# Kernel tuning notes

Measured on AMD Instinct MI355X. Metric: run time of the kernel, lower is better.

The kernel has to match this reference:

```python
import jax, jax.numpy as jnp
import numpy as np

B, C, H, W = 512, 1, 280, 280
K, S, F = 28, 28, 10           # kernel, stride, nfilters
HS, WS = 10, 10                # output spatial spans (280/28)
SPAN = HS * WS                 # 100 patch locations
OUT = 10                       # out_channels
DEC_IN = HS * WS * F           # 1000


def setup_inputs() -> dict:
    key = jax.random.key(0)
    k1, k2, k3, k4, k5 = jax.random.split(key, 5)
    x = jax.random.normal(k1, (B, C, H, W), dtype=jnp.float32)
    # locally-connected weights: one kernel per (filter, spatial location), torch layout [F*SPAN, C, K, K]
    conv_w = jax.random.normal(k2, (F * SPAN, C, K, K), dtype=jnp.float32) * 0.02
    conv_b = jax.random.normal(k3, (F * SPAN, C), dtype=jnp.float32) * 0.02
    dec_w = jax.random.normal(k4, (OUT, DEC_IN), dtype=jnp.float32) * 0.02
    dec_b = jax.random.normal(k5, (OUT,), dtype=jnp.float32) * 0.02
    return {"x": x, "conv_w": conv_w, "conv_b": conv_b, "dec_w": dec_w, "dec_b": dec_b}


def reference(x, conv_w, conv_b, dec_w, dec_b):
    # Extract non-overlapping KxK patches (stride == kernel_size, padding == 0):
    # [B,C,H,W] -> [B,C,HS,K,WS,K] -> [B,HS,WS,C,K,K] -> [B,SPAN,C,K,K]
    # matches torch unfold(2).unfold(3) ordering (height span outer, width span inner).
    patches = x.reshape(B, C, HS, K, WS, K).transpose(0, 2, 4, 1, 3, 5)
    patches = patches.reshape(B, SPAN, C, K, K)
    # weight index in torch is f*SPAN + s (x is tiled SPAN-fastest by repeat)
    w = conv_w.reshape(F, SPAN, C, K, K)
    # per-location elementwise mul + reduce over (kh, kw) == batched tiny contraction
    out = jnp.einsum('bscij,fscij->bfsc', patches, w)  # [B,F,SPAN,C]
    out = out + conv_b.reshape(F, SPAN, C)
    out = out.reshape(B, F, HS, WS)  # valid since C == 1 (as in torch view)
    out = jax.nn.relu(out).reshape(B, DEC_IN)
    return out @ dec_w.T + dec_b
```

## Files before the change

kernel.cpp:

```cpp
#include <hip/hip_runtime.h>
#include <hip/hip_bf16.h>

#define HW      280
#define IMG     78400
#define KK      28
#define F_N     10
#define SPAN    100
#define OUT_N   10
#define P_PLANE 512000

typedef short s16x8 __attribute__((ext_vector_type(8)));
typedef float f32x4 __attribute__((ext_vector_type(4)));

__global__ __launch_bounds__(256) void wprep(const float* __restrict__ cw,
                                             unsigned* __restrict__ wbuf) {
  const int idx = blockIdx.x * 256 + (int)threadIdx.x;
  const int k2  = idx & 15;
  const int f   = (idx >> 4) & 15;
  const int rs  = idx >> 8;
  const int r   = rs % 28;
  const int s   = rs / 28;
  unsigned out = 0;
  if (f < F_N) {
    const int k0 = k2 * 2, k1 = k0 + 1;
    const float v0 = (k0 < KK) ? cw[(size_t)(f * SPAN + s) * (KK * KK) + r * KK + k0] : 0.f;
    const float v1 = (k1 < KK) ? cw[(size_t)(f * SPAN + s) * (KK * KK) + r * KK + k1] : 0.f;
    __hip_bfloat162 h2 = __float22bfloat162_rn(make_float2(v0, v1));
    out = *reinterpret_cast<unsigned*>(&h2);
  }
  wbuf[idx] = out;
}

__global__ __launch_bounds__(256, 4) void lcn_conv(
    const float* __restrict__ x, const unsigned short* __restrict__ wbuf,
    float* __restrict__ P) {
  const int bid  = blockIdx.x;
  const int xcd  = bid & 7;
  const int grp  = bid >> 3;
  const int hsrq = xcd + 8 * (grp % 5);
  const int bg   = grp / 5;
  const int hs   = hsrq >> 2;
  const int rq   = hsrq & 3;

  const int tid  = (int)threadIdx.x;
  const int lane = tid & 63;
  const int wid  = tid >> 6;
  const int l15  = lane & 15;
  const int kg   = lane >> 4;

  __shared__ short xl[2][16 * 320];

  for (int i = tid; i < 2 * 160; i += 256) {
    const int buf = i / 160, j = i - buf * 160;
    const int b = j / 10, ws = j - b * 10;
    const int sidx = (b * 320 + ws * 32 + 28) ^ ((b & 7) << 3);
    *reinterpret_cast<short4*>(&xl[buf][sidx]) = make_short4(0, 0, 0, 0);
  }

  const int nun = (wid < 2) ? 3 : 2;
  const int wsl[3] = {wid, wid + 4, wid + 8};

  f32x4 acc[3];
#pragma unroll
  for (int u = 0; u < 3; ++u) acc[u] = (f32x4){0.f, 0.f, 0.f, 0.f};

  const int row0 = hs * KK + rq * 7;
  const float* xbase = x + (size_t)bg * 16 * IMG + (size_t)row0 * HW;

  float4 stg[5];
  auto issue = [&](int r) {
#pragma unroll
    for (int j = 0; j < 5; ++j) {
      const int i = tid + 256 * j;
      if (i < 1120) {
        const int b = i / 70, q = i - b * 70;
        stg[j] = *reinterpret_cast<const float4*>(
            xbase + (size_t)b * IMG + (size_t)r * HW + q * 4);
      }
    }
  };
  auto commit = [&](int buf) {
#pragma unroll
    for (int j = 0; j < 5; ++j) {
      const int i = tid + 256 * j;
      if (i < 1120) {
        const int b = i / 70, q = i - b * 70;
        const int ws = q / 7, c4 = q - ws * 7;
        __hip_bfloat162 h0 = __float22bfloat162_rn(make_float2(stg[j].x, stg[j].y));
        __hip_bfloat162 h1 = __float22bfloat162_rn(make_float2(stg[j].z, stg[j].w));
        const int sidx = (b * 320 + ws * 32 + c4 * 4) ^ ((b & 7) << 3);
        uint2 pk;
        pk.x = *reinterpret_cast<unsigned*>(&h0);
        pk.y = *reinterpret_cast<unsigned*>(&h1);
        *reinterpret_cast<uint2*>(&xl[buf][sidx]) = pk;
      }
    }
  };

  issue(0);
  commit(0);
  __syncthreads();

  for (int r = 0; r < 7; ++r) {
    const int buf = r & 1;
    if (r < 6) issue(r + 1);
    const int rr = rq * 7 + r;
#pragma unroll
    for (int u = 0; u < 3; ++u) {
      if (u < nun) {
        const int ws = wsl[u];
        const int s  = hs * 10 + ws;
        const s16x8 bfr = *reinterpret_cast<const s16x8*>(
            wbuf + (size_t)(s * 28 + rr) * 512 + l15 * 32 + kg * 8);
        const int sidx = (l15 * 320 + ws * 32 + kg * 8) ^ ((l15 & 7) << 3);
        const s16x8 afr = *reinterpret_cast<const s16x8*>(&xl[buf][sidx]);
        acc[u] = __builtin_amdgcn_mfma_f32_16x16x32_bf16(afr, bfr, acc[u], 0, 0, 0);
      }
    }
    if (r < 6) commit(buf ^ 1);
    __syncthreads();
  }

  if (l15 < F_N) {
#pragma unroll
    for (int u = 0; u < 3; ++u) {
      if (u < nun) {
        const int s = hs * 10 + wsl[u];
        float* Pp = P + (size_t)rq * P_PLANE + (size_t)(l15 * SPAN + s) * 512
                      + bg * 16 + kg * 4;
        *reinterpret_cast<float4*>(Pp) =
            make_float4(acc[u][0], acc[u][1], acc[u][2], acc[u][3]);
      }
    }
  }
}

__global__ __launch_bounds__(256) void lcn_dec(
    const float* __restrict__ P, const float* __restrict__ cb,
    const float* __restrict__ dw, float* __restrict__ yp) {
  const int bid    = blockIdx.x;
  const int dchunk = bid >> 3;
  const int bg     = bid & 7;
  const int lane   = threadIdx.x & 63;
  const int swid   = __builtin_amdgcn_readfirstlane((int)(threadIdx.x >> 6));
  const int d0     = dchunk * 40 + swid * 10;

  const float* Pb = P + (size_t)bg * 64 + lane;
  float acc[OUT_N];
#pragma unroll
  for (int o = 0; o < OUT_N; ++o) acc[o] = 0.f;

#pragma unroll
  for (int dd = 0; dd < 10; ++dd) {
    const int d = d0 + dd;
    const float* pd = Pb + (size_t)d * 512;
    const float p = pd[0] + pd[P_PLANE] + pd[2 * (size_t)P_PLANE] + pd[3 * (size_t)P_PLANE];
    const float h = fmaxf(p + cb[d], 0.f);
#pragma unroll
    for (int o = 0; o < OUT_N; ++o)
      acc[o] = fmaf(h, dw[o * 1000 + d], acc[o]);
  }
  float* ypp = yp + (size_t)(dchunk * 4 + swid) * 5120 + bg * 64 + lane;
#pragma unroll
  for (int o = 0; o < OUT_N; ++o) ypp[(size_t)o * 512] = acc[o];
}

__global__ __launch_bounds__(256) void lcn_yred(
    const float* __restrict__ yp, const float* __restrict__ db,
    float* __restrict__ y) {
  const int idx = blockIdx.x * 256 + (int)threadIdx.x;
  const int o = idx >> 9;
  const int b = idx & 511;
  float a = db[o];
#pragma unroll 10
  for (int p = 0; p < 100; ++p) a += yp[(size_t)p * 5120 + idx];
  y[b * OUT_N + o] = a;
}

extern "C" void kernel_launch(void* const* d_in, const int* in_sizes, int n_in,
                              void* d_out, int out_size, void* d_ws, size_t ws_size,
                              hipStream_t stream) {
  const float* x  = (const float*)d_in[0];
  const float* cw = (const float*)d_in[1];
  const float* cb = (const float*)d_in[2];
  const float* dw = (const float*)d_in[3];
  const float* db = (const float*)d_in[4];
  float* y = (float*)d_out;

  float*    P    = (float*)d_ws;
  float*    yp   = P + 4 * (size_t)P_PLANE;
  unsigned* wbuf = (unsigned*)(yp + 100 * 5120);

  wprep   <<<dim3(2800), dim3(256), 0, stream>>>(cw, wbuf);
  lcn_conv<<<dim3(1280), dim3(256), 0, stream>>>(x, (const unsigned short*)wbuf, P);
  lcn_dec <<<dim3(200),  dim3(256), 0, stream>>>(P, cb, dw, yp);
  lcn_yred<<<dim3(20),   dim3(256), 0, stream>>>(yp, db, y);
}
```

Baseline: 47.60 us.

## Double-prefetch input rows in conv, vectorize weight prep, re-partition decoder

```diff
diff --git a/kernel.cpp b/kernel.cpp
--- a/kernel.cpp
+++ b/kernel.cpp
@@ -12,23 +12,31 @@
 typedef short s16x8 __attribute__((ext_vector_type(8)));
 typedef float f32x4 __attribute__((ext_vector_type(4)));
 
+static __device__ __forceinline__ unsigned bits2(__hip_bfloat162 h) {
+  return *reinterpret_cast<unsigned*>(&h);
+}
+
 __global__ __launch_bounds__(256) void wprep(const float* __restrict__ cw,
-                                             unsigned* __restrict__ wbuf) {
+                                             uint4* __restrict__ wbuf4) {
   const int idx = blockIdx.x * 256 + (int)threadIdx.x;
-  const int k2  = idx & 15;
-  const int f   = (idx >> 4) & 15;
-  const int rs  = idx >> 8;
+  const int k8  = idx & 3;
+  const int f   = (idx >> 2) & 15;
+  const int rs  = idx >> 6;
   const int r   = rs % 28;
   const int s   = rs / 28;
-  unsigned out = 0;
+  uint4 out = make_uint4(0, 0, 0, 0);
   if (f < F_N) {
-    const int k0 = k2 * 2, k1 = k0 + 1;
-    const float v0 = (k0 < KK) ? cw[(size_t)(f * SPAN + s) * (KK * KK) + r * KK + k0] : 0.f;
-    const float v1 = (k1 < KK) ? cw[(size_t)(f * SPAN + s) * (KK * KK) + r * KK + k1] : 0.f;
-    __hip_bfloat162 h2 = __float22bfloat162_rn(make_float2(v0, v1));
-    out = *reinterpret_cast<unsigned*>(&h2);
-  }
-  wbuf[idx] = out;
+    const float* base = cw + (size_t)(f * SPAN + s) * (KK * KK) + r * KK + k8 * 8;
+    const float4 a = *reinterpret_cast<const float4*>(base);
+    out.x = bits2(__float22bfloat162_rn(make_float2(a.x, a.y)));
+    out.y = bits2(__float22bfloat162_rn(make_float2(a.z, a.w)));
+    if (k8 < 3) {
+      const float4 c = *reinterpret_cast<const float4*>(base + 4);
+      out.z = bits2(__float22bfloat162_rn(make_float2(c.x, c.y)));
+      out.w = bits2(__float22bfloat162_rn(make_float2(c.z, c.w)));
+    }
+  }
+  wbuf4[idx] = out;
 }
 
 __global__ __launch_bounds__(256, 4) void lcn_conv(
@@ -67,44 +75,43 @@
   const int row0 = hs * KK + rq * 7;
   const float* xbase = x + (size_t)bg * 16 * IMG + (size_t)row0 * HW;
 
-  float4 stg[5];
-  auto issue = [&](int r) {
-#pragma unroll
-    for (int j = 0; j < 5; ++j) {
-      const int i = tid + 256 * j;
-      if (i < 1120) {
-        const int b = i / 70, q = i - b * 70;
-        stg[j] = *reinterpret_cast<const float4*>(
-            xbase + (size_t)b * IMG + (size_t)r * HW + q * 4);
-      }
-    }
-  };
-  auto commit = [&](int buf) {
-#pragma unroll
-    for (int j = 0; j < 5; ++j) {
-      const int i = tid + 256 * j;
-      if (i < 1120) {
-        const int b = i / 70, q = i - b * 70;
-        const int ws = q / 7, c4 = q - ws * 7;
-        __hip_bfloat162 h0 = __float22bfloat162_rn(make_float2(stg[j].x, stg[j].y));
-        __hip_bfloat162 h1 = __float22bfloat162_rn(make_float2(stg[j].z, stg[j].w));
-        const int sidx = (b * 320 + ws * 32 + c4 * 4) ^ ((b & 7) << 3);
-        uint2 pk;
-        pk.x = *reinterpret_cast<unsigned*>(&h0);
-        pk.y = *reinterpret_cast<unsigned*>(&h1);
-        *reinterpret_cast<uint2*>(&xl[buf][sidx]) = pk;
-      }
-    }
-  };
-
-  issue(0);
-  commit(0);
+  float4 stgA[5], stgB[5];
+
+#define ISSUE(STG, R)                                                       \
+  _Pragma("unroll")                                                         \
+  for (int j = 0; j < 5; ++j) {                                             \
+    const int i = tid + 256 * j;                                            \
+    if (i < 1120) {                                                         \
+      const int b = i / 70, q = i - b * 70;                                 \
+      STG[j] = *reinterpret_cast<const float4*>(                            \
+          xbase + (size_t)b * IMG + (size_t)(R) * HW + q * 4);              \
+    }                                                                       \
+  }
+
+#define COMMIT(STG, BUF)                                                    \
+  _Pragma("unroll")                                                         \
+  for (int j = 0; j < 5; ++j) {                                             \
+    const int i = tid + 256 * j;                                            \
+    if (i < 1120) {                                                         \
+      const int b = i / 70, q = i - b * 70;                                 \
+      const int ws = q / 7, c4 = q - ws * 7;                                \
+      const int sidx = (b * 320 + ws * 32 + c4 * 4) ^ ((b & 7) << 3);       \
+      uint2 pk;                                                             \
+      pk.x = bits2(__float22bfloat162_rn(make_float2(STG[j].x, STG[j].y))); \
+      pk.y = bits2(__float22bfloat162_rn(make_float2(STG[j].z, STG[j].w))); \
+      *reinterpret_cast<uint2*>(&xl[BUF][sidx]) = pk;                       \
+    }                                                                       \
+  }
+
+  ISSUE(stgA, 0)
+  ISSUE(stgB, 1)
+  COMMIT(stgA, 0)
   __syncthreads();
 
+#pragma unroll
   for (int r = 0; r < 7; ++r) {
     const int buf = r & 1;
-    if (r < 6) issue(r + 1);
-    const int rr = rq * 7 + r;
+    const int rr  = rq * 7 + r;
 #pragma unroll
     for (int u = 0; u < 3; ++u) {
       if (u < nun) {
@@ -117,7 +124,12 @@
         acc[u] = __builtin_amdgcn_mfma_f32_16x16x32_bf16(afr, bfr, acc[u], 0, 0, 0);
       }
     }
-    if (r < 6) commit(buf ^ 1);
+    if (r < 6) {
+      if (r & 1) { COMMIT(stgA, 0) } else { COMMIT(stgB, 1) }
+    }
+    if (r < 5) {
+      if (r & 1) { ISSUE(stgB, r + 2) } else { ISSUE(stgA, r + 2) }
+    }
     __syncthreads();
   }
 
@@ -135,45 +147,42 @@
   }
 }
 
-__global__ __launch_bounds__(256) void lcn_dec(
+__global__ __launch_bounds__(512) void lcn_dec(
     const float* __restrict__ P, const float* __restrict__ cb,
     const float* __restrict__ dw, float* __restrict__ yp) {
-  const int bid    = blockIdx.x;
-  const int dchunk = bid >> 3;
-  const int bg     = bid & 7;
-  const int lane   = threadIdx.x & 63;
-  const int swid   = __builtin_amdgcn_readfirstlane((int)(threadIdx.x >> 6));
-  const int d0     = dchunk * 40 + swid * 10;
-
-  const float* Pb = P + (size_t)bg * 64 + lane;
+  const int dchunk = blockIdx.x;
+  const int b      = (int)threadIdx.x;
+
+  const float* Pb = P + b;
   float acc[OUT_N];
 #pragma unroll
   for (int o = 0; o < OUT_N; ++o) acc[o] = 0.f;
 
 #pragma unroll
-  for (int dd = 0; dd < 10; ++dd) {
-    const int d = d0 + dd;
+  for (int dd = 0; dd < 20; ++dd) {
+    const int d = dchunk * 20 + dd;
     const float* pd = Pb + (size_t)d * 512;
-    const float p = pd[0] + pd[P_PLANE] + pd[2 * (size_t)P_PLANE] + pd[3 * (size_t)P_PLANE];
+    const float p = pd[0] + pd[P_PLANE] + pd[2 * (size_t)P_PLANE]
+                          + pd[3 * (size_t)P_PLANE];
     const float h = fmaxf(p + cb[d], 0.f);
 #pragma unroll
     for (int o = 0; o < OUT_N; ++o)
       acc[o] = fmaf(h, dw[o * 1000 + d], acc[o]);
   }
-  float* ypp = yp + (size_t)(dchunk * 4 + swid) * 5120 + bg * 64 + lane;
-#pragma unroll
-  for (int o = 0; o < OUT_N; ++o) ypp[(size_t)o * 512] = acc[o];
-}
-
-__global__ __launch_bounds__(256) void lcn_yred(
+#pragma unroll
+  for (int o = 0; o < OUT_N; ++o)
+    yp[(size_t)(dchunk * OUT_N + o) * 512 + b] = acc[o];
+}
+
+__global__ __launch_bounds__(128) void lcn_yred(
     const float* __restrict__ yp, const float* __restrict__ db,
     float* __restrict__ y) {
-  const int idx = blockIdx.x * 256 + (int)threadIdx.x;
+  const int idx = blockIdx.x * 128 + (int)threadIdx.x;
   const int o = idx >> 9;
   const int b = idx & 511;
   float a = db[o];
 #pragma unroll 10
-  for (int p = 0; p < 100; ++p) a += yp[(size_t)p * 5120 + idx];
+  for (int p = 0; p < 50; ++p) a += yp[(size_t)p * 5120 + idx];
   y[b * OUT_N + o] = a;
 }
 
@@ -189,10 +198,10 @@
 
   float*    P    = (float*)d_ws;
   float*    yp   = P + 4 * (size_t)P_PLANE;
-  unsigned* wbuf = (unsigned*)(yp + 100 * 5120);
-
-  wprep   <<<dim3(2800), dim3(256), 0, stream>>>(cw, wbuf);
+  uint4*    wbuf = (uint4*)(yp + 50 * 5120);
+
+  wprep   <<<dim3(700),  dim3(256), 0, stream>>>(cw, wbuf);
   lcn_conv<<<dim3(1280), dim3(256), 0, stream>>>(x, (const unsigned short*)wbuf, P);
-  lcn_dec <<<dim3(200),  dim3(256), 0, stream>>>(P, cb, dw, yp);
-  lcn_yred<<<dim3(20),   dim3(256), 0, stream>>>(yp, db, y);
-}
+  lcn_dec <<<dim3(50),   dim3(512), 0, stream>>>(P, cb, dw, yp);
+  lcn_yred<<<dim3(40),   dim3(128), 0, stream>>>(yp, db, y);
+}
```

Result: faster. 45.33 us (-4.8%).
